# Kernel optimization log

Measured on AMD Instinct MI355X. Metric: run time of the kernel, lower is better.

## Reference

```python
import jax, jax.numpy as jnp
import numpy as np

PATCH_SIZE = 16
HOP_DISTANCE = 7.0


def setup_inputs() -> dict:
    key = jax.random.key(0)
    x = jax.random.normal(key, (1, 1024, 1024), dtype=jnp.float32)
    return {"x": x}


def _patchify(x, p):
    # Faithful replication of F.unfold(kernel=p, stride=p) followed by .view(-1, p, p)
    # on the contiguous [1, C*p*p, L] unfold output (row-major reshape).
    C, H, W = x.shape
    nH, nW = H // p, W // p
    # unfold layout: [C*p*p, L] with element (c*p*p + ki*p + kj, bi*nW + bj)
    cols = x.reshape(C, nH, p, nW, p).transpose(0, 2, 4, 1, 3).reshape(C * p * p, nH * nW)
    # torch .view(-1, p, p) on contiguous [C*p*p, L] == row-major reshape
    return cols.reshape(-1, p, p)  # [N, p, p], N = C * nH * nW


def reference(x):
    p = PATCH_SIZE
    patches = _patchify(x, p)  # [N, p, p]
    # distance(patch_i, patch_j) = norm over dim=1 (rows) -> per-column vector of length p.
    # d2[i, j, k] = sum_r (patches[i, r, k] - patches[j, r, k])**2, via Gram trick.
    sq = jnp.sum(patches * patches, axis=1)                      # [N, p]
    G = jnp.einsum('irk,jrk->ijk', patches, patches)             # [N, N, p]
    d2 = jnp.maximum(sq[:, None, :] + sq[None, :, :] - 2.0 * G, 0.0)
    # A[i, j] = 1 iff all per-column norms <= hop_distance
    A = jnp.all(jnp.sqrt(d2) <= HOP_DISTANCE, axis=-1).astype(jnp.float32)  # [N, N]
    return A
```

## Files before the change

kernel.cpp:

```cpp
#include <hip/hip_runtime.h>


#define NPATCH 4096
#define BT 64
#define KC 2
#define NPH 8
#define RSTRIDE 9

__device__ __forceinline__ int swzrow(int row) {
    return ((row >> 2) + (row >> 5)) & 7;
}

__global__ __launch_bounds__(256, 3) void adj_kernel(const float* __restrict__ x,
                                                     float* __restrict__ A) {
#pragma clang fp contract(off)
    __shared__ float4 Si[BT * RSTRIDE];
    __shared__ float4 Sj[BT * RSTRIDE];
    __shared__ float sqs[2][KC][BT];

    int t = blockIdx.x;
    int bi = (int)((sqrtf(8.0f * (float)t + 1.0f) - 1.0f) * 0.5f);
    while ((bi + 1) * (bi + 2) / 2 <= t) ++bi;
    while (bi * (bi + 1) / 2 > t) --bi;
    int bj = t - bi * (bi + 1) / 2;

    const int i0 = bi * BT;
    const int j0 = bj * BT;
    const int tid = threadIdx.x;
    const int tx = tid & 15;
    const int ty = tid >> 4;
    const int swzA = (ty + (ty >> 3)) & 7;
    const int swzB = (tx + (tx >> 3)) & 7;

    float m[4][4];
#pragma unroll
    for (int u = 0; u < 4; ++u)
#pragma unroll
        for (int v = 0; v < 4; ++v) m[u][v] = -3.0e38f;

    for (int kp = 0; kp < NPH; ++kp) {
        __syncthreads();
#pragma unroll
        for (int l = 0; l < 4; ++l) {
            int gid = l * 256 + tid;
            int side = gid >> 9;
            int q = gid & 511;
            int kl = q & 1;
            int r = (q >> 1) & 15;
            int rl = q >> 5;
            int k = kp * KC + kl;
            int b = side ? bj : bi;
            int h = rl * 64 + (r >> 2) * 16 + (b >> 2);
            int w0 = (r & 3) * 256 + k * 16 + ((4 * b) & 15);
            float4 v = *(const float4*)&x[h * 1024 + w0];
            const float* vp = (const float*)&v;
            int c = (kl << 2) | (r >> 2);
            int e = r & 3;
            float* Sb = side ? (float*)Sj : (float*)Si;
#pragma unroll
            for (int dd = 0; dd < 4; ++dd) {
                int row = 16 * dd + rl;
                int ch = c ^ swzrow(row);
                Sb[(row * RSTRIDE + ch) * 4 + e] = vp[dd];
            }
        }
        __syncthreads();
        {
            int side = tid >> 7;
            int kl = (tid >> 6) & 1;
            int row = tid & 63;
            const float4* Sb = (side ? Sj : Si) + row * RSTRIDE;
            int swz = swzrow(row);
            float acc;
            {
                float4 v = Sb[(kl * 4) ^ swz];
                acc = v.x * v.x;
                float t1 = v.y * v.y; acc = acc + t1;
                float t2 = v.z * v.z; acc = acc + t2;
                float t3 = v.w * v.w; acc = acc + t3;
            }
#pragma unroll
            for (int rc = 1; rc < 4; ++rc) {
                float4 v = Sb[(kl * 4 + rc) ^ swz];
                float t0 = v.x * v.x; acc = acc + t0;
                float t1 = v.y * v.y; acc = acc + t1;
                float t2 = v.z * v.z; acc = acc + t2;
                float t3 = v.w * v.w; acc = acc + t3;
            }
            sqs[side][kl][row] = acc;
        }
        __syncthreads();
#pragma unroll
        for (int kl = 0; kl < KC; ++kl) {
            float d[4][4];
#pragma unroll
            for (int u = 0; u < 4; ++u)
#pragma unroll
                for (int v = 0; v < 4; ++v) d[u][v] = 0.0f;
#pragma unroll
            for (int rc = 0; rc < 4; ++rc) {
                int c = kl * 4 + rc;
                float4 a[4], b[4];
#pragma unroll
                for (int u = 0; u < 4; ++u)
                    a[u] = Si[(ty * 4 + u) * RSTRIDE + (c ^ swzA)];
#pragma unroll
                for (int v = 0; v < 4; ++v)
                    b[v] = Sj[(tx * 4 + v) * RSTRIDE + (c ^ swzB)];
#pragma unroll
                for (int u = 0; u < 4; ++u)
#pragma unroll
                    for (int v = 0; v < 4; ++v) {
                        d[u][v] = fmaf(a[u].x, b[v].x, d[u][v]);
                        d[u][v] = fmaf(a[u].y, b[v].y, d[u][v]);
                        d[u][v] = fmaf(a[u].z, b[v].z, d[u][v]);
                        d[u][v] = fmaf(a[u].w, b[v].w, d[u][v]);
                    }
            }
            float4 si4 = *(const float4*)&sqs[0][kl][ty * 4];
            float4 sj4 = *(const float4*)&sqs[1][kl][tx * 4];
            const float* sip = (const float*)&si4;
            const float* sjp = (const float*)&sj4;
#pragma unroll
            for (int u = 0; u < 4; ++u)
#pragma unroll
                for (int v = 0; v < 4; ++v) {
                    float s = sip[u] + sjp[v];
                    float d2 = fmaf(-2.0f, d[u][v], s);
                    m[u][v] = fmaxf(m[u][v], d2);
                }
        }
    }

#pragma unroll
    for (int u = 0; u < 4; ++u) {
        float4 o;
        o.x = (m[u][0] <= 49.0f) ? 1.0f : 0.0f;
        o.y = (m[u][1] <= 49.0f) ? 1.0f : 0.0f;
        o.z = (m[u][2] <= 49.0f) ? 1.0f : 0.0f;
        o.w = (m[u][3] <= 49.0f) ? 1.0f : 0.0f;
        *(float4*)&A[(size_t)(i0 + ty * 4 + u) * NPATCH + j0 + tx * 4] = o;
    }
    if (bi != bj) {
#pragma unroll
        for (int v = 0; v < 4; ++v) {
            float4 o;
            o.x = (m[0][v] <= 49.0f) ? 1.0f : 0.0f;
            o.y = (m[1][v] <= 49.0f) ? 1.0f : 0.0f;
            o.z = (m[2][v] <= 49.0f) ? 1.0f : 0.0f;
            o.w = (m[3][v] <= 49.0f) ? 1.0f : 0.0f;
            *(float4*)&A[(size_t)(j0 + tx * 4 + v) * NPATCH + i0 + ty * 4] = o;
        }
    }
}

extern "C" void kernel_launch(void* const* d_in, const int* in_sizes, int n_in,
                              void* d_out, int out_size, void* d_ws, size_t ws_size,
                              hipStream_t stream) {
    const float* x = (const float*)d_in[0];
    float* A = (float*)d_out;
    (void)d_ws; (void)ws_size;

    const int nblk = (NPATCH / BT) * (NPATCH / BT + 1) / 2;
    adj_kernel<<<nblk, 256, 0, stream>>>(x, A);
}
```

Baseline: 154.0 us.

## Pre-transpose patches into workspace and compute adjacency from global loads

Adds a transpose kernel that rearranges the input into a [k][r][n] layout in workspace, plus a separate kernel that precomputes per-column squared norms. The adjacency kernel then reads contiguous float4 vectors directly from global/L2 memory, with no LDS staging and no barriers, and tracks threshold violations as a bitmask instead of a running max. The goal is to remove shared-memory traffic and synchronisation from the main loop. The cost is two extra kernel launches and more global-memory reads that depend on cache hits. The new path is used only when the workspace is large enough.

```diff
diff --git a/kernel.cpp b/kernel.cpp
--- a/kernel.cpp
+++ b/kernel.cpp
@@ -3,6 +3,120 @@
 
 #define NPATCH 4096
 #define BT 64
+
+
+__global__ __launch_bounds__(256) void transpose_kernel(const float* __restrict__ x,
+                                                        float* __restrict__ P2) {
+    int gid = blockIdx.x * 256 + threadIdx.x;
+    int nl = gid & 15;
+    int c  = (gid >> 4) & 3;
+    int n8 = (gid >> 6) & 15;
+    int r  = (gid >> 10) & 15;
+    int k  = gid >> 14;
+    int h = nl * 64 + (r >> 2) * 16 + n8;
+    int w0 = (r & 3) * 256 + k * 16 + 4 * c;
+    float4 v = *(const float4*)&x[h * 1024 + w0];
+    const float* vp = (const float*)&v;
+    float* dst = P2 + (((k * 16 + r) << 12) | (n8 << 8) | nl);
+#pragma unroll
+    for (int j = 0; j < 4; ++j)
+        dst[(4 * c + j) << 4] = vp[j];
+}
+
+__global__ __launch_bounds__(256) void sq2_kernel(const float* __restrict__ P2,
+                                                  float* __restrict__ sq) {
+#pragma clang fp contract(off)
+    int gid = blockIdx.x * 256 + threadIdx.x;
+    int n = gid & 4095;
+    int k = gid >> 12;
+    const float* p = P2 + ((k * 16) << 12) + n;
+    float v0 = p[0];
+    float acc = v0 * v0;
+#pragma unroll
+    for (int r = 1; r < 16; ++r) {
+        float v = p[r << 12];
+        float t = v * v;
+        acc = acc + t;
+    }
+    sq[(k << 12) + n] = acc;
+}
+
+__global__ __launch_bounds__(256, 4) void adj2_kernel(const float* __restrict__ P2,
+                                                      const float* __restrict__ sq,
+                                                      float* __restrict__ A) {
+#pragma clang fp contract(off)
+    int t = blockIdx.x;
+    int bi = (int)((sqrtf(8.0f * (float)t + 1.0f) - 1.0f) * 0.5f);
+    while ((bi + 1) * (bi + 2) / 2 <= t) ++bi;
+    while (bi * (bi + 1) / 2 > t) --bi;
+    int bj = t - bi * (bi + 1) / 2;
+
+    const int i0 = bi * BT;
+    const int j0 = bj * BT;
+    const int tid = threadIdx.x;
+    const int tx = tid & 15;
+    const int ty = tid >> 4;
+    const int ia = i0 + 4 * ty;
+    const int ja = j0 + 4 * tx;
+
+    unsigned int bad = 0u;
+
+    for (int k = 0; k < 16; ++k) {
+        const float* base = P2 + (k << 16);
+        float d[4][4];
+#pragma unroll
+        for (int u = 0; u < 4; ++u)
+#pragma unroll
+            for (int v = 0; v < 4; ++v) d[u][v] = 0.0f;
+#pragma unroll
+        for (int r = 0; r < 16; ++r) {
+            float4 a4 = *(const float4*)&base[(r << 12) + ia];
+            float4 b4 = *(const float4*)&base[(r << 12) + ja];
+            const float* ap = (const float*)&a4;
+            const float* bp = (const float*)&b4;
+#pragma unroll
+            for (int u = 0; u < 4; ++u)
+#pragma unroll
+                for (int v = 0; v < 4; ++v)
+                    d[u][v] = fmaf(ap[u], bp[v], d[u][v]);
+        }
+        float4 si4 = *(const float4*)&sq[(k << 12) + ia];
+        float4 sj4 = *(const float4*)&sq[(k << 12) + ja];
+        const float* sip = (const float*)&si4;
+        const float* sjp = (const float*)&sj4;
+#pragma unroll
+        for (int u = 0; u < 4; ++u)
+#pragma unroll
+            for (int v = 0; v < 4; ++v) {
+                float s = sip[u] + sjp[v];
+                float d2 = fmaf(-2.0f, d[u][v], s);
+                bad |= (d2 > 49.0f) ? (1u << (u * 4 + v)) : 0u;
+            }
+    }
+
+#pragma unroll
+    for (int u = 0; u < 4; ++u) {
+        float4 o;
+        o.x = (bad >> (u * 4 + 0)) & 1u ? 0.0f : 1.0f;
+        o.y = (bad >> (u * 4 + 1)) & 1u ? 0.0f : 1.0f;
+        o.z = (bad >> (u * 4 + 2)) & 1u ? 0.0f : 1.0f;
+        o.w = (bad >> (u * 4 + 3)) & 1u ? 0.0f : 1.0f;
+        *(float4*)&A[(size_t)(i0 + ty * 4 + u) * NPATCH + j0 + tx * 4] = o;
+    }
+    if (bi != bj) {
+#pragma unroll
+        for (int v = 0; v < 4; ++v) {
+            float4 o;
+            o.x = (bad >> (0 * 4 + v)) & 1u ? 0.0f : 1.0f;
+            o.y = (bad >> (1 * 4 + v)) & 1u ? 0.0f : 1.0f;
+            o.z = (bad >> (2 * 4 + v)) & 1u ? 0.0f : 1.0f;
+            o.w = (bad >> (3 * 4 + v)) & 1u ? 0.0f : 1.0f;
+            *(float4*)&A[(size_t)(j0 + tx * 4 + v) * NPATCH + i0 + ty * 4] = o;
+        }
+    }
+}
+
+
 #define KC 2
 #define NPH 8
 #define RSTRIDE 9
@@ -159,8 +273,17 @@
                               hipStream_t stream) {
     const float* x = (const float*)d_in[0];
     float* A = (float*)d_out;
-    (void)d_ws; (void)ws_size;
 
     const int nblk = (NPATCH / BT) * (NPATCH / BT + 1) / 2;
-    adj_kernel<<<nblk, 256, 0, stream>>>(x, A);
-}
+    const size_t need = (size_t)4 * 1024 * 1024 + 256 * 1024;
+
+    if (ws_size >= need) {
+        float* P2 = (float*)d_ws;
+        float* sq = (float*)((char*)d_ws + (size_t)4 * 1024 * 1024);
+        transpose_kernel<<<1024, 256, 0, stream>>>(x, P2);
+        sq2_kernel<<<256, 256, 0, stream>>>(P2, sq);
+        adj2_kernel<<<nblk, 256, 0, stream>>>(P2, sq, A);
+    } else {
+        adj_kernel<<<nblk, 256, 0, stream>>>(x, A);
+    }
+}
```

Result: slower. 233.3 us (+51.5%).
